# Kernel tuning notes

Measured on AMD Instinct MI355X. Metric: run time of the kernel, lower is better.

The kernel has to match this reference:

```python
import jax, jax.numpy as jnp
import numpy as np

N = 64
DX0 = np.pi / N
B = 4096
N_ENV = 8
CODE = 128


def setup_inputs() -> dict:
    key = jax.random.key(0)
    k1, k2, k3 = jax.random.split(key, 3)
    y0 = jax.random.normal(k1, (B, 1, N, N), dtype=jnp.float32)
    env = jax.random.randint(k2, (B,), 0, N_ENV).astype(jnp.int64)
    codes = jax.random.normal(k3, (B, CODE), dtype=jnp.float32)
    t = jnp.zeros((1,), dtype=jnp.float32)
    # learned params: [mu, domain_placeholder] per env (matches nn.Parameter init)
    params = jnp.concatenate([jnp.full((N_ENV, 1), 0.005, jnp.float32),
                              jnp.full((N_ENV, 1), 1.0, jnp.float32)], axis=1)
    # fixed domain buffer for n_env == 8
    domain = jnp.array([0.75, 1.0, 0.75, 1.0, 0.75, 1.0, 0.75, 1.0],
                       dtype=jnp.float32)[:, None]  # [n_env, 1]
    return {"t": t, "y0": y0, "env": env, "codes": codes,
            "params": params, "domain": domain}


def _dx(a):  # roll along last axis (torch dims=2 on [B,H,W])
    return jnp.roll(a, -1, axis=2) - jnp.roll(a, 1, axis=2)


def _dy(a):  # roll along axis 1
    return jnp.roll(a, -1, axis=1) - jnp.roll(a, 1, axis=1)


def _laplacian2d(a, fdx2):
    # torch conv2d (cross-correlation) with kernel [[0,1,0],[1,-4,1],[1,1,0]]
    # and circular padding; note the asymmetric bottom row (faithful to source).
    lap = (jnp.roll(a, 1, axis=1)                    # a[i-1, j]
           + jnp.roll(a, 1, axis=2)                  # a[i, j-1]
           - 4.0 * a
           + jnp.roll(a, -1, axis=2)                 # a[i, j+1]
           + jnp.roll(jnp.roll(a, -1, axis=1), 1, axis=2)  # a[i+1, j-1]
           + jnp.roll(a, -1, axis=1))                # a[i+1, j]
    return lap / fdx2


def _poisson_solve(w, fdx):
    # w: [B,N,N]; fdx: [B,1] grid spacing per sample
    w_pad = jnp.pad(w, ((0, 0), (0, 1), (0, 1)), mode='wrap')  # [B,N+1,N+1]
    wf = jnp.fft.fft2(w_pad / (N ** 2))
    base = jnp.fft.fftfreq(N + 1).astype(w.dtype)       # fftfreq(n, d) = base / d
    k = (2.0 * np.pi) * base[None, :] / fdx             # [B, N+1]
    k2 = k[:, :, None] ** 2 + k[:, None, :] ** 2        # [B, N+1, N+1]
    uf = -wf / (1e-12 + k2)
    uf = uf.at[:, 0, 0].set(0.0)
    return jnp.fft.ifft2((N ** 2) * uf).real[:, :N, :N]


def reference(t, y0, env, codes, params, domain):
    x = y0[:, 0]                              # [B,N,N]
    p = params[env]                           # [B,2]
    mu = p[:, 0:1][..., None]                 # [B,1,1]
    fdx = domain[env] * DX0                   # [B,1]
    psi = _poisson_solve(-x, fdx)             # [B,N,N]
    fdx2 = (fdx[..., None]) ** 2              # [B,1,1]

    rxm = jnp.roll(x, -1, axis=2); rxp = jnp.roll(x, 1, axis=2)
    rym = jnp.roll(x, -1, axis=1); ryp = jnp.roll(x, 1, axis=1)
    pxm = jnp.roll(psi, -1, axis=2); pxp = jnp.roll(psi, 1, axis=2)
    pym = jnp.roll(psi, -1, axis=1); pyp = jnp.roll(psi, 1, axis=1)

    J1 = (_dy(psi) * _dx(x) - _dx(psi) * _dy(x)) / (4.0 * fdx2)
    J2 = (rxm * _dy(pxm) - rxp * _dy(pxp)
          - rym * _dx(pym) + ryp * _dx(pyp)) / (4.0 * fdx2)
    J3 = (jnp.roll(rxm, -1, axis=1) * (pym - pxm)
          - jnp.roll(rxp, 1, axis=1) * (pxp - pyp)
          - jnp.roll(rxp, -1, axis=1) * (pym - pxp)
          + jnp.roll(rxm, 1, axis=1) * (pxm - pyp)) / (4.0 * fdx2)

    dudt = -(J1 + J2 + J3) / 3.0 + mu * _laplacian2d(x, fdx2)
    return dudt[:, None]                      # [B,1,N,N]
```

## Files before the change

kernel.cpp:

```cpp
#include <hip/hip_runtime.h>
#include <math.h>


typedef _Float16 half8 __attribute__((ext_vector_type(8)));
typedef _Float16 half4 __attribute__((ext_vector_type(4)));
typedef float floatx4 __attribute__((ext_vector_type(4)));

#define WPI 0.09666439165562847f

#define H_TB1 0
#define H_TA2 10240
#define H_TG  20480
#define H_TH  26624
#define F_GR32 16384
#define F_GI32 16432
#define F_HC32 16480
#define F_HS32 16528
#define F_SE   16576
#define F_SEG  (F_SE + 264)

#define ARENA 40448
#define OFF_YT   0
#define OFF_XR   0
#define OFF_XI   9216
#define OFF_X32R 18432
#define OFF_X32I 18688
#define OFF_ST   18944
#define OFF_S32  37952
#define OFF_PSIT 18944

__device__ __forceinline__ float trig65(int t, int isSin) {
    return isSin ? __sinf(WPI * (float)t) : __cosf(WPI * (float)t);
}

__global__ void setup_tables(float* __restrict__ ws, const float* __restrict__ domain) {
    int idx = blockIdx.x * 256 + threadIdx.x;
    _Float16* tbH = (_Float16*)ws;
    const float inv = 1.0f / 4225.0f;
    if (idx < 32768) {
        float v = 0.0f;
        int part;
        if (idx < 10240) {
            int chunk = idx >> 9, within = idx & 511;
            part = chunk & 1; int kc = (chunk >> 1) & 1, ni = chunk >> 2;
            int l2 = within >> 3, j = within & 7;
            int row = 16 * ni + (l2 & 15);
            int k = 32 * kc + 8 * (l2 >> 4) + j;
            if (row < 66) {
                int c = (row < 32) ? row : (row < 64 ? row - 32 : 32);
                int isS = (row < 32) ? 0 : (row < 64 ? 1 : row - 64);
                v = trig65((k * c) % 65, isS);
                if (k == 0) v += trig65((64 * c) % 65, isS);
            }
        } else if (idx < 20480) {
            int i2 = idx - 10240;
            int chunk = i2 >> 9, within = i2 & 511;
            part = chunk & 1; int kc = (chunk >> 1) & 1, mi = chunk >> 2;
            int l2 = within >> 3, j = within & 7;
            int row = 16 * mi + (l2 & 15);
            int m = 32 * kc + 8 * (l2 >> 4) + j;
            if (row < 66) {
                int jr = (row < 32) ? row : (row < 64 ? row - 32 : 32);
                int isS = (row < 32) ? 0 : (row < 64 ? 1 : row - 64);
                float s = isS ? 1.0f : -1.0f;
                v = s * trig65((jr * m) % 65, isS);
                if (m == 0) v += s * trig65((jr * 64) % 65, isS);
            }
        } else if (idx < 26624) {
            int i2 = idx - 20480;
            int chunk = i2 >> 9, within = i2 & 511;
            part = chunk & 1; int g = (chunk >> 1) & 1, si = chunk >> 2;
            int l2 = within >> 3, j = within & 7;
            int s = 16 * si + (l2 & 15);
            int jj = 8 * (l2 >> 4) + j;
            if (s <= 32) v = trig65((s * jj) % 65, g);
        } else {
            int i2 = idx - 26624;
            int chunk = i2 >> 9, within = i2 & 511;
            part = chunk & 1; int h = (chunk >> 1) & 1, pi2 = chunk >> 2;
            int l2 = within >> 3, j = within & 7;
            int p = 16 * pi2 + (l2 & 15);
            int c = 8 * (l2 >> 4) + j;
            if (p <= 32) {
                if (c == 0) v = h ? 0.0f : inv;
                else v = 2.0f * inv * trig65((c * p) % 65, h);
            }
        }
        _Float16 hh = (_Float16)v;
        tbH[idx] = part ? (_Float16)(v - (float)hh) : hh;
    } else if (idx < 32960) {
        int i2 = idx - 32768;
        int grp = i2 / 48, s = i2 - grp * 48;
        float v = 0.0f;
        if (s <= 32) {
            int t = (32 * s) % 65;
            float cs = __cosf(WPI * t), sn = __sinf(WPI * t);
            v = (grp == 0) ? cs : (grp == 1) ? sn : (grp == 2) ? 2.0f * inv * cs : 2.0f * inv * sn;
        }
        ws[F_GR32 + i2] = v;
    } else if (idx < 41672) {
        int i2 = idx - 32960;
        const float DX0 = 0.04908738521234052f;
        int e2, a, b2;
        if (i2 < 264) { e2 = i2 / 33; a = i2 - e2 * 33; b2 = 32; }
        else {
            int i3 = i2 - 264;
            e2 = i3 / 1056;
            int rem = i3 - e2 * 1056;
            a = rem >> 5; b2 = rem & 31;
        }
        float fdx = domain[e2] * DX0;
        float tt = 6.283185307179586f / (65.0f * fdx);
        float s2v = tt * tt;
        ws[F_SE + i2] = -1.0f / (1e-12f + s2v * (float)(a * a + b2 * b2));
    }
}

#define MFMA16(A, B, C) __builtin_amdgcn_mfma_f32_16x16x32_f16((A), (B), (C), 0, 0, 0)

__global__ __launch_bounds__(512, 4)
void turb_kernel(const float* __restrict__ y0, const int* __restrict__ env,
                 const float* __restrict__ params, const float* __restrict__ domain,
                 const float* __restrict__ ws, float* __restrict__ out) {
    __shared__ __align__(16) char lds_raw[2 * ARENA];

    const int b0 = blockIdx.x * 2, tid = threadIdx.x;
    const int wid = __builtin_amdgcn_readfirstlane(tid >> 6);
    const int lane = tid & 63, n16 = lane & 15, q = lane >> 4;
    const int lane8 = lane * 8;
    const _Float16* tbH = (const _Float16*)ws;
    const float* tf = ws;

    const int eA0 = __builtin_amdgcn_readfirstlane(env[b0]);
    const int eA1 = __builtin_amdgcn_readfirstlane(env[b0 + 1]);
    const float* SegA[2] = {tf + F_SEG + eA0 * 1056, tf + F_SEG + eA1 * 1056};
    const float* Se3A[2] = {tf + F_SE + eA0 * 33,   tf + F_SE + eA1 * 33};
    const float* xA[2]   = {y0 + (size_t)b0 * 4096,  y0 + (size_t)(b0 + 1) * 4096};
    float* outA[2]       = {out + (size_t)b0 * 4096, out + (size_t)(b0 + 1) * 4096};
    const float DX0 = 0.04908738521234052f;
    float invfA[2], inv12A[2];
    {
        float mu0 = params[2 * eA0], mu1 = params[2 * eA1];
        float f0 = domain[eA0] * DX0, f1 = domain[eA1] * DX0;
        float f02 = f0 * f0, f12 = f1 * f1;
        inv12A[0] = 1.0f / (12.0f * f02); invfA[0] = mu0 / f02;
        inv12A[1] = 1.0f / (12.0f * f12); invfA[1] = mu1 / f12;
    }

    {
        const int mi = wid & 3;
        half8 Ah[2][2], Al[2][2];
        #pragma unroll
        for (int t = 0; t < 2; t++) {
            const float* xrow = xA[t] + (16 * mi + n16) * 64 + 8 * q;
            #pragma unroll
            for (int kc = 0; kc < 2; kc++) {
                float4 v0 = *(const float4*)(xrow + 32 * kc);
                float4 v1 = *(const float4*)(xrow + 32 * kc + 4);
                float vv[8] = {v0.x, v0.y, v0.z, v0.w, v1.x, v1.y, v1.z, v1.w};
                #pragma unroll
                for (int u = 0; u < 8; u++) {
                    _Float16 h = (_Float16)vv[u];
                    Ah[t][kc][u] = h; Al[t][kc][u] = (_Float16)(vv[u] - (float)h);
                }
            }
        }
        const int niBeg = (wid & 4) ? 3 : 0;
        const int niEnd = (wid & 4) ? 5 : 3;
        for (int ni = niBeg; ni < niEnd; ni++) {
            const _Float16* tb = tbH + H_TB1 + ni * 2048 + lane8;
            half8 B0h = *(const half8*)(tb);
            half8 B0l = *(const half8*)(tb + 512);
            half8 B1h = *(const half8*)(tb + 1024);
            half8 B1l = *(const half8*)(tb + 1536);
            const int cp = 16 * ni + n16;
            const bool st = (ni < 4 || n16 < 2);
            #pragma unroll
            for (int t = 0; t < 2; t++) {
                floatx4 acc = {0.f, 0.f, 0.f, 0.f};
                acc = MFMA16(Ah[t][0], B0h, acc); acc = MFMA16(Ah[t][0], B0l, acc); acc = MFMA16(Al[t][0], B0h, acc);
                acc = MFMA16(Ah[t][1], B1h, acc); acc = MFMA16(Ah[t][1], B1l, acc); acc = MFMA16(Al[t][1], B1h, acc);
                if (st) {
                    half4 hh, ll;
                    #pragma unroll
                    for (int i = 0; i < 4; i++) {
                        _Float16 h = (_Float16)acc[i];
                        hh[i] = h; ll[i] = (_Float16)(acc[i] - (float)h);
                    }
                    _Float16* Yt = (_Float16*)(lds_raw + t * ARENA + OFF_YT);
                    *(half4*)(Yt + cp * 136 + 16 * mi + 4 * q) = hh;
                    *(half4*)(Yt + cp * 136 + 64 + 16 * mi + 4 * q) = ll;
                }
            }
        }
    }
    __syncthreads();

    for (int pos = wid; pos < 25; pos += 8) {
        const int mi = pos / 5, ni = pos - 5 * mi;
        const _Float16* ta = tbH + H_TA2 + mi * 2048 + lane8;
        half8 Ah0 = *(const half8*)(ta);
        half8 Al0 = *(const half8*)(ta + 512);
        half8 Ah1 = *(const half8*)(ta + 1024);
        half8 Al1 = *(const half8*)(ta + 1536);
        const int yoff = (16 * ni + n16) * 136 + 8 * q;
        const int cp = 16 * ni + n16;
        const int cc = (ni == 4) ? 32 : (cp & 31);
        const int isS = (ni == 4) ? n16 : (ni >> 1);
        const bool valid = (ni < 4) || (n16 < 2);
        #pragma unroll
        for (int t = 0; t < 2; t++) {
            const _Float16* Yt = (const _Float16*)(lds_raw + t * ARENA + OFF_YT);
            const _Float16* yrow = Yt + yoff;
            half8 Bh0 = *(const half8*)(yrow);
            half8 Bl0 = *(const half8*)(yrow + 64);
            half8 Bh1 = *(const half8*)(yrow + 32);
            half8 Bl1 = *(const half8*)(yrow + 96);
            floatx4 acc = {0.f, 0.f, 0.f, 0.f};
            acc = MFMA16(Ah0, Bh0, acc); acc = MFMA16(Ah0, Bl0, acc); acc = MFMA16(Al0, Bh0, acc);
            acc = MFMA16(Ah1, Bh1, acc); acc = MFMA16(Ah1, Bl1, acc); acc = MFMA16(Al1, Bh1, acc);
            if (valid) {
                _Float16* ST = (_Float16*)(lds_raw + t * ARENA + OFF_ST);
                float* S32 = (float*)(lds_raw + t * ARENA + OFF_S32);
                if (mi < 4) {
                    const int isQ = mi >> 1;
                    const int sid = isQ ? (isS ? 3 : 1) : (isS ? 2 : 0);
                    const int jjb = 16 * (mi & 1) + 4 * q;
                    floatx4 Sv = *(const floatx4*)(SegA[t] + cc * 32 + jjb);
                    float ssg = (sid == 2) ? -2.0f : 2.0f;
                    half4 hh, ll;
                    #pragma unroll
                    for (int i = 0; i < 4; i++) {
                        float v = ssg * Sv[i] * acc[i];
                        _Float16 h = (_Float16)v;
                        hh[i] = h; ll[i] = (_Float16)(v - (float)h);
                    }
                    _Float16* sb = ST + sid * 2376 + cc * 72 + jjb;
                    *(half4*)sb = hh;
                    *(half4*)(sb + 32) = ll;
                } else if (q == 0) {
                    float S = Se3A[t][cc];
                    #pragma unroll
                    for (int i = 0; i < 2; i++) {
                        int sid = i ? (isS ? 3 : 1) : (isS ? 2 : 0);
                        float v = 2.0f * S * acc[i];
                        if (sid == 2) v = -v;
                        S32[sid * 36 + cc] = v;
                    }
                }
            }
        }
    }
    __syncthreads();

    if (wid < 2 && lane < 33) {
        _Float16* ST = (_Float16*)(lds_raw + wid * ARENA + OFF_ST);
        const int c = lane;
        float v0[4];
        #pragma unroll
        for (int sid = 0; sid < 4; sid++)
            v0[sid] = (float)ST[sid * 2376 + c * 72] + (float)ST[sid * 2376 + c * 72 + 32];
        float pr = 0.5f * (v0[0] + v0[3]), pi = 0.5f * (v0[1] + v0[2]);
        if (c == 0) { pr = 0.f; pi = 0.f; }
        float outs[4] = {pr, pi, pi, pr};
        #pragma unroll
        for (int sid = 0; sid < 4; sid++) {
            _Float16 h = (_Float16)outs[sid];
            ST[sid * 2376 + c * 72] = h;
            ST[sid * 2376 + c * 72 + 32] = (_Float16)(outs[sid] - (float)h);
        }
    }
    __syncthreads();

    for (int pos = wid; pos < 18; pos += 8) {
        const int ci = pos / 6, rem = pos - 6 * ci;
        const int si = rem >> 1, g = rem & 1;
        const _Float16* tg = tbH + H_TG + si * 2048 + lane8;
        half8 Grh = *(const half8*)(tg);
        half8 Grl = *(const half8*)(tg + 512);
        half8 Gih = *(const half8*)(tg + 1024);
        half8 Gil = *(const half8*)(tg + 1536);
        const int s = 16 * si + n16;
        const float ga = tf[F_GR32 + s], gi2 = tf[F_GI32 + s];
        const bool sval = (si < 2) || (n16 == 0);
        const float sgn = g ? 1.0f : -1.0f;
        const int cb = 16 * ci + 4 * q;
        const int aoff = (2 * g) * 2376 + (16 * ci + n16) * 72 + 8 * q;
        #pragma unroll
        for (int t = 0; t < 2; t++) {
            const _Float16* ST = (const _Float16*)(lds_raw + t * ARENA + OFF_ST);
            const float* S32 = (const float*)(lds_raw + t * ARENA + OFF_S32);
            const _Float16* st0 = ST + aoff;
            half8 A0h = *(const half8*)(st0),        A0l = *(const half8*)(st0 + 32);
            half8 A1h = *(const half8*)(st0 + 2376), A1l = *(const half8*)(st0 + 2376 + 32);
            floatx4 aA = {0.f,0.f,0.f,0.f}, aB = aA;
            aA = MFMA16(A0h, Grh, aA); aA = MFMA16(A0h, Grl, aA); aA = MFMA16(A0l, Grh, aA);
            aB = MFMA16(A1h, Gih, aB); aB = MFMA16(A1h, Gil, aB); aB = MFMA16(A1l, Gih, aB);
            _Float16* Xo = (_Float16*)(lds_raw + t * ARENA + (g ? OFF_XI : OFF_XR));
            float* X32o = (float*)(lds_raw + t * ARENA + (g ? OFF_X32I : OFF_X32R));
            if (ci < 2) {
                floatx4 U0 = *(const floatx4*)(S32 + (2 * g) * 36 + cb);
                floatx4 U1 = *(const floatx4*)(S32 + (2 * g + 1) * 36 + cb);
                half4 hP, lP, hM, lM;
                #pragma unroll
                for (int i = 0; i < 4; i++) {
                    float av = aA[i] + ga * U0[i], bv = aB[i] + gi2 * U1[i];
                    float xP = av + sgn * bv;
                    float xM = av - sgn * bv;
                    _Float16 h;
                    h = (_Float16)xP; hP[i] = h; lP[i] = (_Float16)(xP - (float)h);
                    h = (_Float16)xM; hM[i] = h; lM[i] = (_Float16)(xM - (float)h);
                }
                if (sval) {
                    *(half4*)(Xo + s * 72 + cb) = hP;  *(half4*)(Xo + s * 72 + 32 + cb) = lP;
                    if (s >= 2) {
                        int sm = 65 - s;
                        *(half4*)(Xo + sm * 72 + cb) = hM;  *(half4*)(Xo + sm * 72 + 32 + cb) = lM;
                    }
                }
            } else if (q == 0 && sval) {
                float u0 = S32[(2 * g) * 36 + 32], u1 = S32[(2 * g + 1) * 36 + 32];
                float av = aA[0] + ga * u0, bv = aB[0] + gi2 * u1;
                X32o[s] = av + sgn * bv;
                if (s >= 2) X32o[65 - s] = av - sgn * bv;
            }
        }
    }
    __syncthreads();

    for (int p24 = wid; p24 < 24; p24 += 8) {
        const int t = p24 / 12;
        const int pos = p24 - 12 * t;
        const int ri = pos / 3, pti = pos - 3 * ri;
        const char* base = lds_raw + t * ARENA;
        const _Float16* Xr = (const _Float16*)(base + OFF_XR);
        const _Float16* Xi = (const _Float16*)(base + OFF_XI);
        const float* X32r = (const float*)(base + OFF_X32R);
        const float* X32i = (const float*)(base + OFF_X32I);
        float* psiT = (float*)(base + OFF_PSIT);
        const int brow = (16 * ri + n16) * 72 + 8 * q;
        half8 Brh = *(const half8*)(Xr + brow), Brl = *(const half8*)(Xr + brow + 32);
        half8 Bih = *(const half8*)(Xi + brow), Bil = *(const half8*)(Xi + brow + 32);
        const _Float16* th = tbH + H_TH + pti * 2048 + lane8;
        half8 Hch = *(const half8*)(th);
        half8 Hcl = *(const half8*)(th + 512);
        half8 Hsh = *(const half8*)(th + 1024);
        half8 Hsl = *(const half8*)(th + 1536);
        floatx4 aE = {0.f,0.f,0.f,0.f}, aF = aE;
        aE = MFMA16(Hch, Brh, aE); aE = MFMA16(Hch, Brl, aE); aE = MFMA16(Hcl, Brh, aE);
        aF = MFMA16(Hsh, Bih, aF); aF = MFMA16(Hsh, Bil, aF); aF = MFMA16(Hsl, Bih, aF);
        const int r = 16 * ri + n16;
        float xr32 = X32r[r], xi32 = X32i[r];
        if (pti < 2) {
            const int pb = 16 * pti + 4 * q;
            floatx4 Hc4 = *(const floatx4*)(tf + F_HC32 + pb);
            floatx4 Hs4 = *(const floatx4*)(tf + F_HS32 + pb);
            float* pp = psiT + pb * 65 + r;
            float* pm = psiT + (65 - pb) * 65 + r;
            #pragma unroll
            for (int i = 0; i < 4; i++) {
                float E = aE[i] + xr32 * Hc4[i];
                float F = aF[i] + xi32 * Hs4[i];
                pp[i * 65] = E - F;
                if (pb + i >= 2) pm[-i * 65] = E + F;
            }
        } else if (q == 0) {
            float E = aE[0] + xr32 * tf[F_HC32 + 32];
            float F = aF[0] + xi32 * tf[F_HS32 + 32];
            psiT[32 * 65 + r] = E - F;
            psiT[33 * 65 + r] = E + F;
        }
    }
    __syncthreads();

    #pragma unroll
    for (int t = 0; t < 2; t++) {
        const float* psiT = (const float*)(lds_raw + t * ARENA + OFF_PSIT);
        const float* x0 = xA[t];
        const float inv12 = inv12A[t], invf = invfA[t];
        const int c = lane;
        const int cm1 = (c + 63) & 63, cp1 = (c + 1) & 63;
        const int r0 = wid * 8;
        const float* xL = x0 + r0 * 64 + cm1;
        const float* xC = x0 + r0 * 64 + c;
        const float* xR = x0 + r0 * 64 + cp1;
        const float* pL = psiT + cm1 * 65 + r0;
        const float* pC = psiT + c * 65 + r0;
        const float* pR = psiT + cp1 * 65 + r0;
        float* ob = outA[t] + r0 * 64 + c;
        const int mo = (wid == 0) ? 63 : -1;
        float xLm = xL[mo * 64], xCm = xC[mo * 64], xRm = xR[mo * 64];
        float pLm = pL[mo], pCm = pC[mo], pRm = pR[mo];
        float xLc = xL[0], xCc = xC[0], xRc = xR[0];
        float pLc = pL[0], pCc = pC[0], pRc = pR[0];
        #pragma unroll
        for (int it = 0; it < 8; it++) {
            int ro = it + 1;
            if (it == 7 && wid == 7) ro = -56;
            float xLp = xL[ro * 64], xCp = xC[ro * 64], xRp = xR[ro * 64];
            float pLp = pL[ro], pCp = pC[ro], pRp = pR[ro];
            float J1 = (pCp - pCm) * (xRc - xLc) - (pRc - pLc) * (xCp - xCm);
            float J2 = xRc * (pRp - pRm) - xLc * (pLp - pLm) - xCp * (pRp - pLp) + xCm * (pRm - pLm);
            float J3 = xRp * (pCp - pRc) - xLm * (pLc - pCm) - xLp * (pCp - pLc) + xRm * (pRc - pCm);
            float lap = xCm + xLc - 4.f * xCc + xRc + xLp + xCp;
            ob[it * 64] = -(J1 + J2 + J3) * inv12 + lap * invf;
            xLm = xLc; xCm = xCc; xRm = xRc; pLm = pLc; pCm = pCc; pRm = pRc;
            xLc = xLp; xCc = xCp; xRc = xRp; pLc = pLp; pCc = pCp; pRc = pRp;
        }
    }
}

extern "C" void kernel_launch(void* const* d_in, const int* in_sizes, int n_in,
                              void* d_out, int out_size, void* d_ws, size_t ws_size,
                              hipStream_t stream) {
    const float* y0     = (const float*)d_in[1];
    const int*   env    = (const int*)d_in[2];
    const float* params = (const float*)d_in[4];
    const float* domain = (const float*)d_in[5];
    float* out = (float*)d_out;
    float* ws  = (float*)d_ws;

    setup_tables<<<dim3(163), dim3(256), 0, stream>>>(ws, domain);
    turb_kernel<<<dim3(2048), dim3(512), 0, stream>>>(y0, env, params, domain, ws, out);
}
```

Measured before the change: 179.9 us.

## Process four samples per block and prefetch next DFT table tile

Each block now handles four samples (NB=4) instead of two, so the LDS arena grows to four slots and the grid halves. Every DFT/twiddle table fragment loaded from global memory is reused across more samples. The second-stage loop also prefetches the next position's TA2 fragments into registers before the current MFMAs run. In exchange, the LDS footprint nearly fills the CU's local memory, so likely only one block fits per CU, and register pressure rises from holding four samples' split-fp16 operands.

```diff
diff --git a/kernel.cpp b/kernel.cpp
--- a/kernel.cpp
+++ b/kernel.cpp
@@ -20,6 +20,7 @@
 #define F_SEG  (F_SE + 264)
 
 #define ARENA 40448
+#define NB 4
 #define OFF_YT   0
 #define OFF_XR   0
 #define OFF_XI   9216
@@ -118,40 +119,42 @@
 
 #define MFMA16(A, B, C) __builtin_amdgcn_mfma_f32_16x16x32_f16((A), (B), (C), 0, 0, 0)
 
-__global__ __launch_bounds__(512, 4)
+__global__ __launch_bounds__(512, 2)
 void turb_kernel(const float* __restrict__ y0, const int* __restrict__ env,
                  const float* __restrict__ params, const float* __restrict__ domain,
                  const float* __restrict__ ws, float* __restrict__ out) {
-    __shared__ __align__(16) char lds_raw[2 * ARENA];
-
-    const int b0 = blockIdx.x * 2, tid = threadIdx.x;
+    __shared__ __align__(16) char lds_raw[NB * ARENA];
+
+    const int b0 = blockIdx.x * NB, tid = threadIdx.x;
     const int wid = __builtin_amdgcn_readfirstlane(tid >> 6);
     const int lane = tid & 63, n16 = lane & 15, q = lane >> 4;
     const int lane8 = lane * 8;
     const _Float16* tbH = (const _Float16*)ws;
     const float* tf = ws;
 
-    const int eA0 = __builtin_amdgcn_readfirstlane(env[b0]);
-    const int eA1 = __builtin_amdgcn_readfirstlane(env[b0 + 1]);
-    const float* SegA[2] = {tf + F_SEG + eA0 * 1056, tf + F_SEG + eA1 * 1056};
-    const float* Se3A[2] = {tf + F_SE + eA0 * 33,   tf + F_SE + eA1 * 33};
-    const float* xA[2]   = {y0 + (size_t)b0 * 4096,  y0 + (size_t)(b0 + 1) * 4096};
-    float* outA[2]       = {out + (size_t)b0 * 4096, out + (size_t)(b0 + 1) * 4096};
+    int eA[NB];
+    const float *SegA[NB], *Se3A[NB], *xA[NB];
+    float* outA[NB];
+    float invfA[NB], inv12A[NB];
     const float DX0 = 0.04908738521234052f;
-    float invfA[2], inv12A[2];
-    {
-        float mu0 = params[2 * eA0], mu1 = params[2 * eA1];
-        float f0 = domain[eA0] * DX0, f1 = domain[eA1] * DX0;
-        float f02 = f0 * f0, f12 = f1 * f1;
-        inv12A[0] = 1.0f / (12.0f * f02); invfA[0] = mu0 / f02;
-        inv12A[1] = 1.0f / (12.0f * f12); invfA[1] = mu1 / f12;
+    #pragma unroll
+    for (int t = 0; t < NB; t++) {
+        eA[t] = __builtin_amdgcn_readfirstlane(env[b0 + t]);
+        SegA[t] = tf + F_SEG + eA[t] * 1056;
+        Se3A[t] = tf + F_SE + eA[t] * 33;
+        xA[t]   = y0 + (size_t)(b0 + t) * 4096;
+        outA[t] = out + (size_t)(b0 + t) * 4096;
+        float mu = params[2 * eA[t]];
+        float f = domain[eA[t]] * DX0, f2 = f * f;
+        inv12A[t] = 1.0f / (12.0f * f2);
+        invfA[t] = mu / f2;
     }
 
     {
         const int mi = wid & 3;
-        half8 Ah[2][2], Al[2][2];
+        half8 Ah[NB][2], Al[NB][2];
         #pragma unroll
-        for (int t = 0; t < 2; t++) {
+        for (int t = 0; t < NB; t++) {
             const float* xrow = xA[t] + (16 * mi + n16) * 64 + 8 * q;
             #pragma unroll
             for (int kc = 0; kc < 2; kc++) {
@@ -176,7 +179,7 @@
             const int cp = 16 * ni + n16;
             const bool st = (ni < 4 || n16 < 2);
             #pragma unroll
-            for (int t = 0; t < 2; t++) {
+            for (int t = 0; t < NB; t++) {
                 floatx4 acc = {0.f, 0.f, 0.f, 0.f};
                 acc = MFMA16(Ah[t][0], B0h, acc); acc = MFMA16(Ah[t][0], B0l, acc); acc = MFMA16(Al[t][0], B0h, acc);
                 acc = MFMA16(Ah[t][1], B1h, acc); acc = MFMA16(Ah[t][1], B1l, acc); acc = MFMA16(Al[t][1], B1h, acc);
@@ -196,64 +199,81 @@
     }
     __syncthreads();
 
-    for (int pos = wid; pos < 25; pos += 8) {
-        const int mi = pos / 5, ni = pos - 5 * mi;
-        const _Float16* ta = tbH + H_TA2 + mi * 2048 + lane8;
-        half8 Ah0 = *(const half8*)(ta);
-        half8 Al0 = *(const half8*)(ta + 512);
-        half8 Ah1 = *(const half8*)(ta + 1024);
-        half8 Al1 = *(const half8*)(ta + 1536);
-        const int yoff = (16 * ni + n16) * 136 + 8 * q;
-        const int cp = 16 * ni + n16;
-        const int cc = (ni == 4) ? 32 : (cp & 31);
-        const int isS = (ni == 4) ? n16 : (ni >> 1);
-        const bool valid = (ni < 4) || (n16 < 2);
-        #pragma unroll
-        for (int t = 0; t < 2; t++) {
-            const _Float16* Yt = (const _Float16*)(lds_raw + t * ARENA + OFF_YT);
-            const _Float16* yrow = Yt + yoff;
-            half8 Bh0 = *(const half8*)(yrow);
-            half8 Bl0 = *(const half8*)(yrow + 64);
-            half8 Bh1 = *(const half8*)(yrow + 32);
-            half8 Bl1 = *(const half8*)(yrow + 96);
-            floatx4 acc = {0.f, 0.f, 0.f, 0.f};
-            acc = MFMA16(Ah0, Bh0, acc); acc = MFMA16(Ah0, Bl0, acc); acc = MFMA16(Al0, Bh0, acc);
-            acc = MFMA16(Ah1, Bh1, acc); acc = MFMA16(Ah1, Bl1, acc); acc = MFMA16(Al1, Bh1, acc);
-            if (valid) {
-                _Float16* ST = (_Float16*)(lds_raw + t * ARENA + OFF_ST);
-                float* S32 = (float*)(lds_raw + t * ARENA + OFF_S32);
-                if (mi < 4) {
-                    const int isQ = mi >> 1;
-                    const int sid = isQ ? (isS ? 3 : 1) : (isS ? 2 : 0);
-                    const int jjb = 16 * (mi & 1) + 4 * q;
-                    floatx4 Sv = *(const floatx4*)(SegA[t] + cc * 32 + jjb);
-                    float ssg = (sid == 2) ? -2.0f : 2.0f;
-                    half4 hh, ll;
-                    #pragma unroll
-                    for (int i = 0; i < 4; i++) {
-                        float v = ssg * Sv[i] * acc[i];
-                        _Float16 h = (_Float16)v;
-                        hh[i] = h; ll[i] = (_Float16)(v - (float)h);
-                    }
-                    _Float16* sb = ST + sid * 2376 + cc * 72 + jjb;
-                    *(half4*)sb = hh;
-                    *(half4*)(sb + 32) = ll;
-                } else if (q == 0) {
-                    float S = Se3A[t][cc];
-                    #pragma unroll
-                    for (int i = 0; i < 2; i++) {
-                        int sid = i ? (isS ? 3 : 1) : (isS ? 2 : 0);
-                        float v = 2.0f * S * acc[i];
-                        if (sid == 2) v = -v;
-                        S32[sid * 36 + cc] = v;
+    {
+        int pos = wid;
+        half8 Ah0, Al0, Ah1, Al1;
+        {
+            const _Float16* ta = tbH + H_TA2 + (pos / 5) * 2048 + lane8;
+            Ah0 = *(const half8*)(ta);
+            Al0 = *(const half8*)(ta + 512);
+            Ah1 = *(const half8*)(ta + 1024);
+            Al1 = *(const half8*)(ta + 1536);
+        }
+        while (pos < 25) {
+            const int mi = pos / 5, ni = pos - 5 * mi;
+            const int npos = pos + 8;
+            half8 nAh0 = {}, nAl0 = {}, nAh1 = {}, nAl1 = {};
+            if (npos < 25) {
+                const _Float16* ta = tbH + H_TA2 + (npos / 5) * 2048 + lane8;
+                nAh0 = *(const half8*)(ta);
+                nAl0 = *(const half8*)(ta + 512);
+                nAh1 = *(const half8*)(ta + 1024);
+                nAl1 = *(const half8*)(ta + 1536);
+            }
+            const int yoff = (16 * ni + n16) * 136 + 8 * q;
+            const int cp = 16 * ni + n16;
+            const int cc = (ni == 4) ? 32 : (cp & 31);
+            const int isS = (ni == 4) ? n16 : (ni >> 1);
+            const bool valid = (ni < 4) || (n16 < 2);
+            #pragma unroll
+            for (int t = 0; t < NB; t++) {
+                const _Float16* Yt = (const _Float16*)(lds_raw + t * ARENA + OFF_YT);
+                const _Float16* yrow = Yt + yoff;
+                half8 Bh0 = *(const half8*)(yrow);
+                half8 Bl0 = *(const half8*)(yrow + 64);
+                half8 Bh1 = *(const half8*)(yrow + 32);
+                half8 Bl1 = *(const half8*)(yrow + 96);
+                floatx4 acc = {0.f, 0.f, 0.f, 0.f};
+                acc = MFMA16(Ah0, Bh0, acc); acc = MFMA16(Ah0, Bl0, acc); acc = MFMA16(Al0, Bh0, acc);
+                acc = MFMA16(Ah1, Bh1, acc); acc = MFMA16(Ah1, Bl1, acc); acc = MFMA16(Al1, Bh1, acc);
+                if (valid) {
+                    _Float16* ST = (_Float16*)(lds_raw + t * ARENA + OFF_ST);
+                    float* S32 = (float*)(lds_raw + t * ARENA + OFF_S32);
+                    if (mi < 4) {
+                        const int isQ = mi >> 1;
+                        const int sid = isQ ? (isS ? 3 : 1) : (isS ? 2 : 0);
+                        const int jjb = 16 * (mi & 1) + 4 * q;
+                        floatx4 Sv = *(const floatx4*)(SegA[t] + cc * 32 + jjb);
+                        float ssg = (sid == 2) ? -2.0f : 2.0f;
+                        half4 hh, ll;
+                        #pragma unroll
+                        for (int i = 0; i < 4; i++) {
+                            float v = ssg * Sv[i] * acc[i];
+                            _Float16 h = (_Float16)v;
+                            hh[i] = h; ll[i] = (_Float16)(v - (float)h);
+                        }
+                        _Float16* sb = ST + sid * 2376 + cc * 72 + jjb;
+                        *(half4*)sb = hh;
+                        *(half4*)(sb + 32) = ll;
+                    } else if (q == 0) {
+                        float S = Se3A[t][cc];
+                        #pragma unroll
+                        for (int i = 0; i < 2; i++) {
+                            int sid = i ? (isS ? 3 : 1) : (isS ? 2 : 0);
+                            float v = 2.0f * S * acc[i];
+                            if (sid == 2) v = -v;
+                            S32[sid * 36 + cc] = v;
+                        }
                     }
                 }
             }
+            Ah0 = nAh0; Al0 = nAl0; Ah1 = nAh1; Al1 = nAl1;
+            pos = npos;
         }
     }
     __syncthreads();
 
-    if (wid < 2 && lane < 33) {
+    if (wid < NB && lane < 33) {
         _Float16* ST = (_Float16*)(lds_raw + wid * ARENA + OFF_ST);
         const int c = lane;
         float v0[4];
@@ -287,7 +307,7 @@
         const int cb = 16 * ci + 4 * q;
         const int aoff = (2 * g) * 2376 + (16 * ci + n16) * 72 + 8 * q;
         #pragma unroll
-        for (int t = 0; t < 2; t++) {
+        for (int t = 0; t < NB; t++) {
             const _Float16* ST = (const _Float16*)(lds_raw + t * ARENA + OFF_ST);
             const float* S32 = (const float*)(lds_raw + t * ARENA + OFF_S32);
             const _Float16* st0 = ST + aoff;
@@ -328,9 +348,9 @@
     }
     __syncthreads();
 
-    for (int p24 = wid; p24 < 24; p24 += 8) {
-        const int t = p24 / 12;
-        const int pos = p24 - 12 * t;
+    for (int p48 = wid; p48 < 48; p48 += 8) {
+        const int t = p48 / 12;
+        const int pos = p48 - 12 * t;
         const int ri = pos / 3, pti = pos - 3 * ri;
         const char* base = lds_raw + t * ARENA;
         const _Float16* Xr = (const _Float16*)(base + OFF_XR);
@@ -374,7 +394,7 @@
     __syncthreads();
 
     #pragma unroll
-    for (int t = 0; t < 2; t++) {
+    for (int t = 0; t < NB; t++) {
         const float* psiT = (const float*)(lds_raw + t * ARENA + OFF_PSIT);
         const float* x0 = xA[t];
         const float inv12 = inv12A[t], invf = invfA[t];
@@ -421,5 +441,5 @@
     float* ws  = (float*)d_ws;
 
     setup_tables<<<dim3(163), dim3(256), 0, stream>>>(ws, domain);
-    turb_kernel<<<dim3(2048), dim3(512), 0, stream>>>(y0, env, params, domain, ws, out);
+    turb_kernel<<<dim3(1024), dim3(512), 0, stream>>>(y0, env, params, domain, ws, out);
 }
```

Measured after the change: 198.9 us. 10.5% more time.
